# Optimization experiments

Measured on AMD Instinct MI355X. Metric: run time of the kernel, lower is better.

## Reference

```python
import jax, jax.numpy as jnp
import numpy as np

G = 4          # conv groups (hardcoded in module)
C = 1024       # channels (hardcoded cin=cout=1024)
SCALE = 1.0 / np.sqrt(1024.0).astype(np.float32)  # 1/sqrt(c/h), h=1


def grouped_proj(x, W, b):
    # pointwise grouped Conv1d == block-diagonal matmul over channel groups
    # x: [B, C, P], W: [G, C//G out, C//G in], b: [C]
    B, C_, P = x.shape
    xg = x.reshape(B, G, C_ // G, P)
    y = jnp.einsum('goi,bgip->bgop', W, xg)  # [B, G, C//G, P]
    return y.reshape(B, C_, P) + b[None, :, None]


def setup_inputs() -> dict:
    key = jax.random.key(0)
    ks = jax.random.split(key, 8)
    B, PK, PQ = 8, 1024, 4096
    cg = C // G
    w_std = 1.0 / np.sqrt(cg).astype(np.float32)  # ~ conv default init scale
    return {
        'Xq': jax.random.normal(ks[0], (B, C, PQ), jnp.float32),
        'Xk': jax.random.normal(ks[1], (B, C, PK), jnp.float32),
        'Wq': jax.random.normal(ks[2], (G, cg, cg), jnp.float32) * w_std,
        'bq': jax.random.normal(ks[3], (C,), jnp.float32) * 0.01,
        'Wk': jax.random.normal(ks[4], (G, cg, cg), jnp.float32) * w_std,
        'bk': jax.random.normal(ks[5], (C,), jnp.float32) * 0.01,
        'Wv': jax.random.normal(ks[6], (G, cg, cg), jnp.float32) * w_std,
        'bv': jax.random.normal(ks[7], (C,), jnp.float32) * 0.01,
    }


def reference(Xq, Xk, Wq, bq, Wk, bk, Wv, bv):
    # Q and K are both projected from Xk; V from Xq (as in the torch code)
    Q = grouped_proj(Xk, Wq, bq)   # [B, C, Pk]
    K = grouped_proj(Xk, Wk, bk)   # [B, C, Pk]
    V = grouped_proj(Xq, Wv, bv)   # [B, C, Pq]
    b, c, pk = K.shape
    pq = V.shape[-1]
    h = 1
    Qh = Q.reshape(b, h, c // h, pk)
    Kh = K.reshape(b, h, c // h, pk)
    Vh = V.reshape(b, h, c // h, pq)
    # H: [B, h, Pk, Pq], contraction over channels; softmax over dim=-2 (Pk)
    H = jnp.einsum('bhci,bhcj->bhij', Kh, Vh) * SCALE
    H = jax.nn.softmax(H, axis=-2)
    # sparse_constrain: Gram over last axis vs identity, mean squared error
    mid = jnp.einsum('bhci,bhki->bhck', H, H)          # [B, h, Pk, Pk]
    Iden = jnp.eye(pk, dtype=H.dtype)[None, None]       # broadcast over B, h
    sparse_loss = jnp.mean((mid - Iden) ** 2)
    # out: mix Q along Pk with attention H -> [B, h, C, Pq]
    out = jnp.einsum('bhij,bhki->bhkj', H, Qh).reshape(b, c, pq)
    return out, sparse_loss, H
```

## Files before the change

kernel.cpp:

```cpp
#include <hip/hip_runtime.h>

typedef _Float16 f16;
typedef f16 f16x4 __attribute__((ext_vector_type(4)));
typedef f16 f16x8 __attribute__((ext_vector_type(8)));
typedef float f32x4 __attribute__((ext_vector_type(4)));

__device__ __forceinline__ void gload16(const void* g, void* ldsbase) {
  __builtin_amdgcn_global_load_lds((const __attribute__((address_space(1))) unsigned int*)g,
                                   (__attribute__((address_space(3))) unsigned int*)ldsbase, 16, 0, 0);
}

__device__ __forceinline__ int swz(int row, int c) {
  return row * 64 + ((c ^ ((row >> 1) & 3)) << 4);
}

template<int MODE>
__global__ void __launch_bounds__(512, 2)
gemm256(const f16* __restrict__ A, const f16* __restrict__ Bm, float* __restrict__ Cf,
        f16* __restrict__ E16, f16* __restrict__ E16t,
        int K, long sA, long sB, float scale, float* __restrict__ aux) {
  __shared__ f16 sb[65536];
  const int t = threadIdx.x, l = t & 63, w = t >> 6;
  const int wr = w >> 2, wc = w & 3;
  const int bid = blockIdx.x;
  const int swzb = (bid & 7) * 64 + (bid >> 3);
  const long b = swzb >> 6;
  const int inner = swzb & 63;
  const int bx = inner >> 2, by = inner & 3;
  const char* Abyte = (const char*)(A + b * sA + (long)(by * 256) * K);
  const char* Bbyte = (const char*)(Bm + b * sB + (long)(bx * 256) * K);

  int offSrc[4];
#pragma unroll
  for (int i = 0; i < 4; ++i) {
    int cid = i * 512 + t, row = cid >> 3, slot = cid & 7;
    offSrc[i] = row * (K * 2) + ((slot ^ (row & 7)) << 4);
  }
  int offAf[8][2], offBf[4][2];
#pragma unroll
  for (int mi = 0; mi < 8; ++mi) {
    int r = wr * 128 + mi * 16 + (l & 15);
#pragma unroll
    for (int ks = 0; ks < 2; ++ks)
      offAf[mi][ks] = r * 64 + ((((ks << 2) + (l >> 4)) ^ (r & 7)) << 3);
  }
#pragma unroll
  for (int ni = 0; ni < 4; ++ni) {
    int r = wc * 64 + ni * 16 + (l & 15);
#pragma unroll
    for (int ks = 0; ks < 2; ++ks)
      offBf[ni][ks] = r * 64 + ((((ks << 2) + (l >> 4)) ^ (r & 7)) << 3);
  }

  const int NT = K >> 6;
  f32x4 acc[8][4] = {};

  auto STAGE = [&](int kt, int bsel) {
    f16* la = sb + bsel * 32768;
    f16* lb = la + 16384;
    const char* as = Abyte + (long)kt * 128;
    const char* bs = Bbyte + (long)kt * 128;
#pragma unroll
    for (int i = 0; i < 4; ++i)
      gload16(as + offSrc[i], la + (i * 512 + (w << 6)) * 8);
#pragma unroll
    for (int i = 0; i < 4; ++i)
      gload16(bs + offSrc[i], lb + (i * 512 + (w << 6)) * 8);
  };

  STAGE(0, 0);
  for (int kt = 0; kt < NT; ++kt) {
    const int cur = kt & 1;
    if (kt + 1 < NT) {
      STAGE(kt + 1, cur ^ 1);
      asm volatile("s_waitcnt vmcnt(8)" ::: "memory");
    } else {
      asm volatile("s_waitcnt vmcnt(0)" ::: "memory");
    }
    __builtin_amdgcn_s_barrier();
    asm volatile("" ::: "memory");
    const f16* la = sb + cur * 32768;
    const f16* lb = la + 16384;
#pragma unroll
    for (int ks = 0; ks < 2; ++ks) {
      f16x8 bf[4];
#pragma unroll
      for (int ni = 0; ni < 4; ++ni) bf[ni] = *(const f16x8*)(lb + offBf[ni][ks]);
#pragma unroll
      for (int mi = 0; mi < 8; ++mi) {
        f16x8 af = *(const f16x8*)(la + offAf[mi][ks]);
#pragma unroll
        for (int ni = 0; ni < 4; ++ni)
          acc[mi][ni] = __builtin_amdgcn_mfma_f32_16x16x32_f16(af, bf[ni], acc[mi][ni], 0, 0, 0);
      }
    }
    asm volatile("s_waitcnt lgkmcnt(0)" ::: "memory");
    __builtin_amdgcn_s_barrier();
    asm volatile("" ::: "memory");
  }

  const int i0 = by * 256, j0 = bx * 256;
  if (MODE == 2) {
    float csum[4] = {};
#pragma unroll
    for (int mi = 0; mi < 8; ++mi)
#pragma unroll
      for (int ni = 0; ni < 4; ++ni)
#pragma unroll
        for (int q = 0; q < 4; ++q) {
          float e = __expf(acc[mi][ni][q] * scale);
          acc[mi][ni][q] = e;
          csum[ni] += e;
        }
#pragma unroll
    for (int ni = 0; ni < 4; ++ni) {
      csum[ni] += __shfl_xor(csum[ni], 16);
      csum[ni] += __shfl_xor(csum[ni], 32);
    }
    float* colp = (float*)(sb + 34816);
    if (l < 16) {
#pragma unroll
      for (int ni = 0; ni < 4; ++ni) colp[wr * 256 + wc * 64 + ni * 16 + l] = csum[ni];
    }
    __syncthreads();
    if (t < 256) aux[(b * 4 + by) * 4096 + bx * 256 + t] = colp[t] + colp[256 + t];
    f16* E16b = E16 + b * 4194304L;
    f16* E16tb = E16t + b * 4194304L;
#pragma unroll
    for (int s = 0; s < 4; ++s) {
      if (wr == (s >> 1)) {
        const int h = s & 1;
#pragma unroll
        for (int m2 = 0; m2 < 4; ++m2)
#pragma unroll
          for (int ni = 0; ni < 4; ++ni)
#pragma unroll
            for (int q = 0; q < 4; ++q)
              sb[(m2 * 16 + (l >> 4) * 4 + q) * 264 + wc * 64 + ni * 16 + (l & 15)] =
                  (f16)acc[h * 4 + m2][ni][q];
      }
      __syncthreads();
#pragma unroll
      for (int ii = 0; ii < 4; ++ii) {
        int cid = ii * 512 + t, r = cid >> 5, cc = cid & 31;
        *(f16x8*)(E16b + (long)(i0 + s * 64 + r) * 4096 + j0 + cc * 8) =
            *(const f16x8*)(sb + r * 264 + cc * 8);
      }
      const int q4 = w >> 1, r8 = l >> 3, ic = l & 7;
#pragma unroll
      for (int ii = 0; ii < 4; ++ii) {
        int j = q4 * 64 + r8 * 8 + (w & 1) * 4 + ii;
        f16x8 v;
#pragma unroll
        for (int k2 = 0; k2 < 8; ++k2) v[k2] = sb[(ic * 8 + k2) * 264 + j];
        *(f16x8*)(E16tb + (long)(j0 + j) * 1024 + i0 + s * 64 + ic * 8) = v;
      }
      __syncthreads();
    }
  }
}

__global__ void __launch_bounds__(512, 2)
fused3(const f16* __restrict__ Q, const f16* __restrict__ Et, float* __restrict__ Cf,
       const float* __restrict__ invg,
       const f16* __restrict__ E, const f16* __restrict__ inv2sg,
       float* __restrict__ Hf, float* __restrict__ parts) {
  __shared__ f16 sb[69632];
  const int t = threadIdx.x, l = t & 63, w = t >> 6;
  const int wr = w >> 2, wc = w & 3;

  if (blockIdx.x < 80) {
    const int bid = blockIdx.x;
    const long b = bid & 7;
    int by = 0, r = bid >> 3;
    while (r >= 4 - by) { r -= 4 - by; ++by; }
    const int bx = by + r;
    const char* Abyte = (const char*)(E + b * 4194304L + (long)(by * 256) * 4096);
    const char* Bbyte = (const char*)(E + b * 4194304L + (long)(bx * 256) * 4096);
    f16* invl = sb + 65536;
    gload16((const char*)(inv2sg + b * 4096) + (long)t * 16, invl + (w << 6) * 8);
    int offSrc[4];
#pragma unroll
    for (int i = 0; i < 4; ++i) {
      int cid = i * 512 + t, row = cid >> 3, slot = cid & 7;
      offSrc[i] = row * 8192 + ((slot ^ (row & 7)) << 4);
    }
    int offAf[8][2], offBf[4][2];
#pragma unroll
    for (int mi = 0; mi < 8; ++mi) {
      int rr = wr * 128 + mi * 16 + (l & 15);
#pragma unroll
      for (int ks = 0; ks < 2; ++ks)
        offAf[mi][ks] = rr * 64 + ((((ks << 2) + (l >> 4)) ^ (rr & 7)) << 3);
    }
#pragma unroll
    for (int ni = 0; ni < 4; ++ni) {
      int rr = wc * 64 + ni * 16 + (l & 15);
#pragma unroll
      for (int ks = 0; ks < 2; ++ks)
        offBf[ni][ks] = rr * 64 + ((((ks << 2) + (l >> 4)) ^ (rr & 7)) << 3);
    }
    f32x4 acc[8][4] = {};
    auto STAGE = [&](int kt, int bsel) {
      f16* la = sb + bsel * 32768;
      f16* lb = la + 16384;
      const char* as = Abyte + (long)kt * 128;
      const char* bs = Bbyte + (long)kt * 128;
#pragma unroll
      for (int i = 0; i < 4; ++i) gload16(as + offSrc[i], la + (i * 512 + (w << 6)) * 8);
#pragma unroll
      for (int i = 0; i < 4; ++i) gload16(bs + offSrc[i], lb + (i * 512 + (w << 6)) * 8);
    };
    const int kwA = bx * 16;
    const int kwB = by * 16;
    const bool dual = (by != bx);
    STAGE(0, 0);
    for (int kt = 0; kt < 64; ++kt) {
      const int cur = kt & 1;
      if (kt + 1 < 64) {
        STAGE(kt + 1, cur ^ 1);
        const int pk = kt - 1;
        const bool wrote = (pk >= kwA && pk < kwA + 16) || (dual && pk >= kwB && pk < kwB + 16);
        if (wrote) asm volatile("s_waitcnt vmcnt(40)" ::: "memory");
        else       asm volatile("s_waitcnt vmcnt(8)" ::: "memory");
      } else {
        asm volatile("s_waitcnt vmcnt(0)" ::: "memory");
      }
      __builtin_amdgcn_s_barrier();
      asm volatile("" ::: "memory");
      const f16* la = sb + cur * 32768;
      const f16* lb = la + 16384;
#pragma unroll
      for (int ks = 0; ks < 2; ++ks) {
        const f16x8 invv = *(const f16x8*)(invl + kt * 64 + ks * 32 + ((l >> 4) << 3));
        f16x8 bf[4];
#pragma unroll
        for (int ni = 0; ni < 4; ++ni) bf[ni] = *(const f16x8*)(lb + offBf[ni][ks]);
#pragma unroll
        for (int mi = 0; mi < 8; ++mi) {
          f16x8 af = *(const f16x8*)(la + offAf[mi][ks]) * invv;
#pragma unroll
          for (int ni = 0; ni < 4; ++ni)
            acc[mi][ni] = __builtin_amdgcn_mfma_f32_16x16x32_f16(af, bf[ni], acc[mi][ni], 0, 0, 0);
        }
      }
      if (kt >= kwA && kt < kwA + 16) {
        const float iv = sqrtf((float)invl[kt * 64 + l]) * (1.0f / 64.0f);
        float* hp = Hf + b * 4194304L + (long)(by * 256 + w * 32) * 4096 + kt * 64 + l;
#pragma unroll
        for (int rr = 0; rr < 32; ++rr) {
          const int row = w * 32 + rr;
          f16 ev = la[row * 64 + ((((l >> 3) ^ (row & 7)) << 3) | (l & 7))];
          hp[(long)rr * 4096] = (float)ev * iv;
        }
      }
      if (dual && kt >= kwB && kt < kwB + 16) {
        const float iv = sqrtf((float)invl[kt * 64 + l]) * (1.0f / 64.0f);
        float* hp = Hf + b * 4194304L + (long)(bx * 256 + w * 32) * 4096 + kt * 64 + l;
#pragma unroll
        for (int rr = 0; rr < 32; ++rr) {
          const int row = w * 32 + rr;
          f16 ev = lb[row * 64 + ((((l >> 3) ^ (row & 7)) << 3) | (l & 7))];
          hp[(long)rr * 4096] = (float)ev * iv;
        }
      }
      asm volatile("s_waitcnt lgkmcnt(0)" ::: "memory");
      __builtin_amdgcn_s_barrier();
      asm volatile("" ::: "memory");
    }
    const int gr0 = by * 256 + wr * 128 + (l >> 4) * 4;
    const int gc0 = bx * 256 + wc * 64 + (l & 15);
    float p = 0.f;
#pragma unroll
    for (int mi = 0; mi < 8; ++mi)
#pragma unroll
      for (int ni = 0; ni < 4; ++ni)
#pragma unroll
        for (int q = 0; q < 4; ++q) {
          float e = acc[mi][ni][q] * (1.0f / 4096.0f);
          if (gr0 + mi * 16 + q == gc0 + ni * 16) e -= 1.f;
          p += e * e;
        }
    if (dual) p *= 2.f;
#pragma unroll
    for (int d = 32; d; d >>= 1) p += __shfl_down(p, d);
    __shared__ float red[8];
    if (l == 0) red[w] = p;
    __syncthreads();
    if (t == 0) {
      float s = 0.f;
#pragma unroll
      for (int i = 0; i < 8; ++i) s += red[i];
      parts[bid] = s;
    }
  } else {
    const int bid = blockIdx.x - 80;
    const int swzb = (bid & 7) * 64 + (bid >> 3);
    const long b = swzb >> 6;
    const int inner = swzb & 63;
    const int bx = inner >> 2, by = inner & 3;
    const char* Abyte = (const char*)(Q + b * 1048576L + (long)(by * 256) * 1024);
    const char* Bbyte = (const char*)(Et + b * 4194304L + (long)(bx * 256) * 1024);
    int offSrc[4];
#pragma unroll
    for (int i = 0; i < 4; ++i) {
      int cid = i * 512 + t, row = cid >> 3, slot = cid & 7;
      offSrc[i] = row * 2048 + ((slot ^ (row & 7)) << 4);
    }
    int offAf[8][2], offBf[4][2];
#pragma unroll
    for (int mi = 0; mi < 8; ++mi) {
      int r = wr * 128 + mi * 16 + (l & 15);
#pragma unroll
      for (int ks = 0; ks < 2; ++ks)
        offAf[mi][ks] = r * 64 + ((((ks << 2) + (l >> 4)) ^ (r & 7)) << 3);
    }
#pragma unroll
    for (int ni = 0; ni < 4; ++ni) {
      int r = wc * 64 + ni * 16 + (l & 15);
#pragma unroll
      for (int ks = 0; ks < 2; ++ks)
        offBf[ni][ks] = r * 64 + ((((ks << 2) + (l >> 4)) ^ (r & 7)) << 3);
    }
    f32x4 acc[8][4] = {};
    auto STAGE = [&](int kt, int bsel) {
      f16* la = sb + bsel * 32768;
      f16* lb = la + 16384;
      const char* as = Abyte + (long)kt * 128;
      const char* bs = Bbyte + (long)kt * 128;
#pragma unroll
      for (int i = 0; i < 4; ++i) gload16(as + offSrc[i], la + (i * 512 + (w << 6)) * 8);
#pragma unroll
      for (int i = 0; i < 4; ++i) gload16(bs + offSrc[i], lb + (i * 512 + (w << 6)) * 8);
    };
    STAGE(0, 0);
    for (int kt = 0; kt < 16; ++kt) {
      const int cur = kt & 1;
      if (kt + 1 < 16) {
        STAGE(kt + 1, cur ^ 1);
        asm volatile("s_waitcnt vmcnt(8)" ::: "memory");
      } else {
        asm volatile("s_waitcnt vmcnt(0)" ::: "memory");
      }
      __builtin_amdgcn_s_barrier();
      asm volatile("" ::: "memory");
      const f16* la = sb + cur * 32768;
      const f16* lb = la + 16384;
#pragma unroll
      for (int ks = 0; ks < 2; ++ks) {
        f16x8 bf[4];
#pragma unroll
        for (int ni = 0; ni < 4; ++ni) bf[ni] = *(const f16x8*)(lb + offBf[ni][ks]);
#pragma unroll
        for (int mi = 0; mi < 8; ++mi) {
          f16x8 af = *(const f16x8*)(la + offAf[mi][ks]);
#pragma unroll
          for (int ni = 0; ni < 4; ++ni)
            acc[mi][ni] = __builtin_amdgcn_mfma_f32_16x16x32_f16(af, bf[ni], acc[mi][ni], 0, 0, 0);
        }
      }
      asm volatile("s_waitcnt lgkmcnt(0)" ::: "memory");
      __builtin_amdgcn_s_barrier();
      asm volatile("" ::: "memory");
    }
    const float* ip = invg + b * 4096 + bx * 256 + wc * 64;
    float iv[4];
#pragma unroll
    for (int ni = 0; ni < 4; ++ni) iv[ni] = ip[ni * 16 + (l & 15)];
    float* Cb = Cf + b * 4194304L + (long)(by * 256 + wr * 128) * 4096 + bx * 256 + wc * 64;
#pragma unroll
    for (int mi = 0; mi < 8; ++mi)
#pragma unroll
      for (int ni = 0; ni < 4; ++ni)
#pragma unroll
        for (int q = 0; q < 4; ++q)
          Cb[(long)(mi * 16 + (l >> 4) * 4 + q) * 4096 + ni * 16 + (l & 15)] = acc[mi][ni][q] * iv[ni];
  }
}

__global__ void __launch_bounds__(512)
proj_qk(const float* __restrict__ X, const f16* __restrict__ Wq16, const f16* __restrict__ Wk16,
        const float* __restrict__ bq, const float* __restrict__ bk,
        f16* __restrict__ Q, f16* __restrict__ Kt) {
  __shared__ f16 sb[20480];
  f16* Wqs = sb;
  f16* Wks = sb + 8192;
  f16* Xs = sb + 16384;
  const int t = threadIdx.x, l = t & 63, w = t >> 6;
  const int wrq = w >> 1, wcq = w & 1;
  const int bg = blockIdx.z, g = bg & 3;
  const long b = bg >> 2;
  const int p0 = blockIdx.x * 128;
  const float* Xb = X + b * 1048576 + (long)g * 262144;
  const char* WqB = (const char*)(Wq16 + g * 65536);
  const char* WkB = (const char*)(Wk16 + g * 65536);
  int wOff[2];
#pragma unroll
  for (int i = 0; i < 2; ++i) {
    int c = i * 512 + t, row = c >> 2, slot = (c & 3) ^ ((row >> 1) & 3);
    wOff[i] = row * 512 + (slot << 4);
  }
  const int xp = t & 127, xc = t >> 7;
  const float* xS = Xb + (long)(xc * 8) * 1024 + p0 + xp;
  const int xo = swz(xp, xc);
  int offW[4], offX[4];
#pragma unroll
  for (int i = 0; i < 4; ++i) {
    int rc = wrq * 64 + i * 16 + (l & 15);
    offW[i] = swz(rc, l >> 4);
    int rp = wcq * 64 + i * 16 + (l & 15);
    offX[i] = swz(rp, l >> 4);
  }
  f32x4 accq[4][4] = {}, acck[4][4] = {};
  for (int k0 = 0; k0 < 256; k0 += 32) {
#pragma unroll
    for (int i = 0; i < 2; ++i) {
      gload16(WqB + wOff[i] + k0 * 2, Wqs + (i * 512 + (w << 6)) * 8);
      gload16(WkB + wOff[i] + k0 * 2, Wks + (i * 512 + (w << 6)) * 8);
    }
    const float* xs = xS + (long)k0 * 1024;
    f16x8 v;
#pragma unroll
    for (int d = 0; d < 8; ++d) v[d] = (f16)xs[(long)d * 1024];
    *(f16x8*)((char*)Xs + xo) = v;
    __syncthreads();
    f16x8 qf[4], kf[4], xf[4];
#pragma unroll
    for (int i = 0; i < 4; ++i) {
      qf[i] = *(const f16x8*)((const char*)Wqs + offW[i]);
      kf[i] = *(const f16x8*)((const char*)Wks + offW[i]);
      xf[i] = *(const f16x8*)((const char*)Xs + offX[i]);
    }
#pragma unroll
    for (int mi = 0; mi < 4; ++mi)
#pragma unroll
      for (int ni = 0; ni < 4; ++ni) {
        accq[mi][ni] = __builtin_amdgcn_mfma_f32_16x16x32_f16(qf[mi], xf[ni], accq[mi][ni], 0, 0, 0);
        acck[ni][mi] = __builtin_amdgcn_mfma_f32_16x16x32_f16(xf[ni], kf[mi], acck[ni][mi], 0, 0, 0);
      }
    __syncthreads();
  }
  f16* Qb = Q + b * 1048576 + (long)(g * 256 + wrq * 64) * 1024 + p0 + wcq * 64;
#pragma unroll
  for (int mi = 0; mi < 4; ++mi)
#pragma unroll
    for (int q = 0; q < 4; ++q) {
      float bv = bq[g * 256 + wrq * 64 + mi * 16 + (l >> 4) * 4 + q];
#pragma unroll
      for (int ni = 0; ni < 4; ++ni)
        Qb[(long)(mi * 16 + (l >> 4) * 4 + q) * 1024 + ni * 16 + (l & 15)] = (f16)(accq[mi][ni][q] + bv);
    }
  f16* Kb = Kt + b * 1048576 + (long)(p0 + wcq * 64) * 1024 + g * 256 + wrq * 64;
  float bcol[4];
#pragma unroll
  for (int ni = 0; ni < 4; ++ni) bcol[ni] = bk[g * 256 + wrq * 64 + ni * 16 + (l & 15)];
#pragma unroll
  for (int mi = 0; mi < 4; ++mi)
#pragma unroll
    for (int q = 0; q < 4; ++q)
#pragma unroll
      for (int ni = 0; ni < 4; ++ni)
        Kb[(long)(mi * 16 + (l >> 4) * 4 + q) * 1024 + ni * 16 + (l & 15)] = (f16)(acck[mi][ni][q] + bcol[ni]);
}

__global__ void __launch_bounds__(512)
proj_v(const float* __restrict__ X, const f16* __restrict__ Wv16, const float* __restrict__ bv,
       f16* __restrict__ Vt) {
  __shared__ f16 sb[12288];
  f16* Wvs = sb;
  f16* Xs = sb + 8192;
  const int t = threadIdx.x, l = t & 63, w = t >> 6;
  const int wrq = w >> 1, wcq = w & 1;
  const int bg = blockIdx.z, g = bg & 3;
  const long b = bg >> 2;
  const int p0 = blockIdx.x * 128;
  const float* Xb = X + b * 4194304 + (long)g * 1048576;
  const char* WvB = (const char*)(Wv16 + g * 65536);
  int wOff[2];
#pragma unroll
  for (int i = 0; i < 2; ++i) {
    int c = i * 512 + t, row = c >> 2, slot = (c & 3) ^ ((row >> 1) & 3);
    wOff[i] = row * 512 + (slot << 4);
  }
  const int xp = t & 127, xc = t >> 7;
  const float* xS = Xb + (long)(xc * 8) * 4096 + p0 + xp;
  const int xo = swz(xp, xc);
  int offW[4], offX[4];
#pragma unroll
  for (int i = 0; i < 4; ++i) {
    int rc = wrq * 64 + i * 16 + (l & 15);
    offW[i] = swz(rc, l >> 4);
    int rp = wcq * 64 + i * 16 + (l & 15);
    offX[i] = swz(rp, l >> 4);
  }
  f32x4 acc[4][4] = {};
  for (int k0 = 0; k0 < 256; k0 += 32) {
#pragma unroll
    for (int i = 0; i < 2; ++i)
      gload16(WvB + wOff[i] + k0 * 2, Wvs + (i * 512 + (w << 6)) * 8);
    const float* xs = xS + (long)k0 * 4096;
    f16x8 v;
#pragma unroll
    for (int d = 0; d < 8; ++d) v[d] = (f16)xs[(long)d * 4096];
    *(f16x8*)((char*)Xs + xo) = v;
    __syncthreads();
    f16x8 wf[4], xf[4];
#pragma unroll
    for (int i = 0; i < 4; ++i) {
      wf[i] = *(const f16x8*)((const char*)Wvs + offW[i]);
      xf[i] = *(const f16x8*)((const char*)Xs + offX[i]);
    }
#pragma unroll
    for (int mi = 0; mi < 4; ++mi)
#pragma unroll
      for (int ni = 0; ni < 4; ++ni)
        acc[mi][ni] = __builtin_amdgcn_mfma_f32_16x16x32_f16(xf[mi], wf[ni], acc[mi][ni], 0, 0, 0);
    __syncthreads();
  }
  f16* Vb = Vt + b * 4194304 + (long)(p0 + wcq * 64) * 1024 + g * 256 + wrq * 64;
  float bcol[4];
#pragma unroll
  for (int ni = 0; ni < 4; ++ni) bcol[ni] = bv[g * 256 + wrq * 64 + ni * 16 + (l & 15)];
#pragma unroll
  for (int mi = 0; mi < 4; ++mi)
#pragma unroll
    for (int q = 0; q < 4; ++q)
#pragma unroll
      for (int ni = 0; ni < 4; ++ni)
        Vb[(long)(mi * 16 + (l >> 4) * 4 + q) * 1024 + ni * 16 + (l & 15)] = (f16)(acc[mi][ni][q] + bcol[ni]);
}

__global__ void __launch_bounds__(256)
inv_k(const float* __restrict__ colsum, float* __restrict__ inv, f16* __restrict__ inv2s) {
  int gid = blockIdx.x * 256 + threadIdx.x;
  int b = gid >> 12, j = gid & 4095;
  const float* cp = colsum + (long)(b * 4) * 4096 + j;
  float s = 0.f;
#pragma unroll
  for (int my = 0; my < 4; ++my) s += cp[my * 4096];
  float iv = 1.f / s;
  inv[gid] = iv;
  inv2s[gid] = (f16)(iv * iv * 4096.0f);
}

__global__ void cvt3(const float* __restrict__ a, const float* __restrict__ b2,
                     const float* __restrict__ c, f16* __restrict__ da,
                     f16* __restrict__ db, f16* __restrict__ dc) {
  int i = blockIdx.x * 256 + threadIdx.x;
  int which = i >> 18, r = i & 262143;
  if (which == 0) da[r] = (f16)a[r];
  else if (which == 1) db[r] = (f16)b2[r];
  else dc[r] = (f16)c[r];
}

__global__ void __launch_bounds__(256)
finalize_k(const float* __restrict__ parts, float* __restrict__ o) {
  const int t = threadIdx.x;
  float s = (t < 80) ? parts[t] : 0.f;
#pragma unroll
  for (int d = 32; d; d >>= 1) s += __shfl_down(s, d);
  __shared__ float red[4];
  if ((t & 63) == 0) red[t >> 6] = s;
  __syncthreads();
  if (t == 0) *o = (red[0] + red[1] + red[2] + red[3]) * (1.0f / 8388608.0f);
}

extern "C" void kernel_launch(void* const* d_in, const int* in_sizes, int n_in,
                              void* d_out, int out_size, void* d_ws, size_t ws_size,
                              hipStream_t stream) {
  const float* Xq = (const float*)d_in[0];
  const float* Xk = (const float*)d_in[1];
  const float* Wq = (const float*)d_in[2];
  const float* bq = (const float*)d_in[3];
  const float* Wk = (const float*)d_in[4];
  const float* bk = (const float*)d_in[5];
  const float* Wv = (const float*)d_in[6];
  const float* bv = (const float*)d_in[7];
  float* out = (float*)d_out;
  float* loss_out = out + 33554432;
  float* Hf = out + 33554433;

  char* ws = (char*)d_ws;
  f16* W16q = (f16*)(ws);
  f16* W16k = (f16*)(ws + (1 << 19));
  f16* W16v = (f16*)(ws + 2L * (1 << 19));
  f16* Q16  = (f16*)(ws + 3L * (1 << 19));
  f16* Kt16 = (f16*)(ws + 3L * (1 << 19) + (1L << 24));
  f16* Vt16 = (f16*)(ws + 3L * (1 << 19) + 2L * (1 << 24));
  f16* E16  = (f16*)(ws + 3L * (1 << 19) + 2L * (1 << 24) + (1L << 26));
  f16* E16t = (f16*)(ws + 3L * (1 << 19) + 2L * (1 << 24) + 2L * (1 << 26));
  char* tail = ws + 3L * (1 << 19) + 2L * (1 << 24) + 3L * (1 << 26);
  float* parts = (float*)tail;
  float* invb  = (float*)(tail + 8192);
  f16*   inv2s = (f16*)(tail + 8192 + 131072);
  float* colsum = (float*)(ws);

  cvt3<<<3072, 256, 0, stream>>>(Wq, Wk, Wv, W16q, W16k, W16v);

  proj_qk<<<dim3(8, 1, 32), 512, 0, stream>>>(Xk, W16q, W16k, bq, bk, Q16, Kt16);
  proj_v <<<dim3(32, 1, 32), 512, 0, stream>>>(Xq, W16v, bv, Vt16);

  gemm256<2><<<512, 512, 0, stream>>>(Kt16, Vt16, nullptr, E16, E16t,
      1024, 1L << 20, 1L << 22, 0.03125f, colsum);

  inv_k<<<128, 256, 0, stream>>>(colsum, invb, inv2s);

  fused3<<<592, 512, 0, stream>>>(Q16, E16t, out, invb, E16, inv2s, Hf, parts);
  finalize_k<<<1, 256, 0, stream>>>(parts, loss_out);
}
```

Before: 379.8 us.

## Split Gram GEMM K dimension in two and reduce partial tiles separately

The sparse-loss Gram GEMM blocks in the fused kernel now split the 4096-long reduction into two halves, doubling Gram blocks from 80 to 160 so the long-running tail blocks are shorter and load balance with the output GEMM blocks improves. Each half writes its full 256x256 fp32 partial tile to workspace, and a new gram_red kernel sums the halves, subtracts identity and reduces squared error. The H write-out schedule is remapped so each panel is still written exactly once. This adds about 42MB of extra global traffic and one more kernel launch.

Result: faster. 371.3 us, median of 2 (-2.2%).

```diff
diff --git a/kernel.cpp b/kernel.cpp
--- a/kernel.cpp
+++ b/kernel.cpp
@@ -164,19 +164,24 @@
 fused3(const f16* __restrict__ Q, const f16* __restrict__ Et, float* __restrict__ Cf,
        const float* __restrict__ invg,
        const f16* __restrict__ E, const f16* __restrict__ inv2sg,
-       float* __restrict__ Hf, float* __restrict__ parts) {
+       float* __restrict__ Hf, float* __restrict__ midS) {
   __shared__ f16 sb[69632];
   const int t = threadIdx.x, l = t & 63, w = t >> 6;
   const int wr = w >> 2, wc = w & 3;
 
-  if (blockIdx.x < 80) {
+  if (blockIdx.x < 160) {
     const int bid = blockIdx.x;
     const long b = bid & 7;
-    int by = 0, r = bid >> 3;
+    const int rest = bid >> 3;
+    const int h = rest & 1;
+    int by = 0, r = rest >> 1;
     while (r >= 4 - by) { r -= 4 - by; ++by; }
     const int bx = by + r;
-    const char* Abyte = (const char*)(E + b * 4194304L + (long)(by * 256) * 4096);
-    const char* Bbyte = (const char*)(E + b * 4194304L + (long)(bx * 256) * 4096);
+    const char* Abyte = (const char*)(E + b * 4194304L + (long)(by * 256) * 4096 + 2048L * h);
+    const char* Bbyte = (const char*)(E + b * 4194304L + (long)(bx * 256) * 4096 + 2048L * h);
+    const int d = bx - by;
+    const int wA = (d == 1) ? 0 : (d == 2 ? 1 : -1);
+    const int wB = (d == 3) ? 0 : ((d == 1 && by >= 1) ? 1 : -1);
     f16* invl = sb + 65536;
     gload16((const char*)(inv2sg + b * 4096) + (long)t * 16, invl + (w << 6) * 8);
     int offSrc[4];
@@ -201,26 +206,23 @@
         offBf[ni][ks] = rr * 64 + ((((ks << 2) + (l >> 4)) ^ (rr & 7)) << 3);
     }
     f32x4 acc[8][4] = {};
-    auto STAGE = [&](int kt, int bsel) {
+    auto STAGE = [&](int lk, int bsel) {
       f16* la = sb + bsel * 32768;
       f16* lb = la + 16384;
-      const char* as = Abyte + (long)kt * 128;
-      const char* bs = Bbyte + (long)kt * 128;
+      const char* as = Abyte + (long)lk * 128;
+      const char* bs = Bbyte + (long)lk * 128;
 #pragma unroll
       for (int i = 0; i < 4; ++i) gload16(as + offSrc[i], la + (i * 512 + (w << 6)) * 8);
 #pragma unroll
       for (int i = 0; i < 4; ++i) gload16(bs + offSrc[i], lb + (i * 512 + (w << 6)) * 8);
     };
-    const int kwA = bx * 16;
-    const int kwB = by * 16;
-    const bool dual = (by != bx);
     STAGE(0, 0);
-    for (int kt = 0; kt < 64; ++kt) {
-      const int cur = kt & 1;
-      if (kt + 1 < 64) {
-        STAGE(kt + 1, cur ^ 1);
-        const int pk = kt - 1;
-        const bool wrote = (pk >= kwA && pk < kwA + 16) || (dual && pk >= kwB && pk < kwB + 16);
+    for (int lk = 0; lk < 32; ++lk) {
+      const int cur = lk & 1;
+      if (lk + 1 < 32) {
+        STAGE(lk + 1, cur ^ 1);
+        const int ps = (lk - 1) >> 4;
+        const bool wrote = (lk >= 1) && (wA == ps || wB == ps);
         if (wrote) asm volatile("s_waitcnt vmcnt(40)" ::: "memory");
         else       asm volatile("s_waitcnt vmcnt(8)" ::: "memory");
       } else {
@@ -228,11 +230,12 @@
       }
       __builtin_amdgcn_s_barrier();
       asm volatile("" ::: "memory");
+      const int ktg = 32 * h + lk;
       const f16* la = sb + cur * 32768;
       const f16* lb = la + 16384;
 #pragma unroll
       for (int ks = 0; ks < 2; ++ks) {
-        const f16x8 invv = *(const f16x8*)(invl + kt * 64 + ks * 32 + ((l >> 4) << 3));
+        const f16x8 invv = *(const f16x8*)(invl + ktg * 64 + ks * 32 + ((l >> 4) << 3));
         f16x8 bf[4];
 #pragma unroll
         for (int ni = 0; ni < 4; ++ni) bf[ni] = *(const f16x8*)(lb + offBf[ni][ks]);
@@ -244,57 +247,34 @@
             acc[mi][ni] = __builtin_amdgcn_mfma_f32_16x16x32_f16(af, bf[ni], acc[mi][ni], 0, 0, 0);
         }
       }
-      if (kt >= kwA && kt < kwA + 16) {
-        const float iv = sqrtf((float)invl[kt * 64 + l]) * (1.0f / 64.0f);
-        float* hp = Hf + b * 4194304L + (long)(by * 256 + w * 32) * 4096 + kt * 64 + l;
-#pragma unroll
-        for (int rr = 0; rr < 32; ++rr) {
-          const int row = w * 32 + rr;
-          f16 ev = la[row * 64 + ((((l >> 3) ^ (row & 7)) << 3) | (l & 7))];
-          hp[(long)rr * 4096] = (float)ev * iv;
-        }
-      }
-      if (dual && kt >= kwB && kt < kwB + 16) {
-        const float iv = sqrtf((float)invl[kt * 64 + l]) * (1.0f / 64.0f);
-        float* hp = Hf + b * 4194304L + (long)(bx * 256 + w * 32) * 4096 + kt * 64 + l;
-#pragma unroll
-        for (int rr = 0; rr < 32; ++rr) {
-          const int row = w * 32 + rr;
-          f16 ev = lb[row * 64 + ((((l >> 3) ^ (row & 7)) << 3) | (l & 7))];
-          hp[(long)rr * 4096] = (float)ev * iv;
+      const int slot = lk >> 4;
+      if (wA == slot || wB == slot) {
+        const int panel = (wA == slot) ? by : bx;
+        const f16* src = (wA == slot) ? la : lb;
+        const float iv = sqrtf((float)invl[ktg * 64 + l]) * (1.0f / 64.0f);
+        float* hp = Hf + b * 4194304L + (long)(panel * 256 + w * 32) * 4096 + ktg * 64 + l;
+#pragma unroll
+        for (int rr2 = 0; rr2 < 32; ++rr2) {
+          const int row = w * 32 + rr2;
+          f16 ev = src[row * 64 + ((((l >> 3) ^ (row & 7)) << 3) | (l & 7))];
+          hp[(long)rr2 * 4096] = (float)ev * iv;
         }
       }
       asm volatile("s_waitcnt lgkmcnt(0)" ::: "memory");
       __builtin_amdgcn_s_barrier();
       asm volatile("" ::: "memory");
     }
-    const int gr0 = by * 256 + wr * 128 + (l >> 4) * 4;
-    const int gc0 = bx * 256 + wc * 64 + (l & 15);
-    float p = 0.f;
+    float* mt = midS + (long)(((rest >> 1) * 8 + b) * 2 + h) * 65536;
 #pragma unroll
     for (int mi = 0; mi < 8; ++mi)
 #pragma unroll
       for (int ni = 0; ni < 4; ++ni)
 #pragma unroll
-        for (int q = 0; q < 4; ++q) {
-          float e = acc[mi][ni][q] * (1.0f / 4096.0f);
-          if (gr0 + mi * 16 + q == gc0 + ni * 16) e -= 1.f;
-          p += e * e;
-        }
-    if (dual) p *= 2.f;
-#pragma unroll
-    for (int d = 32; d; d >>= 1) p += __shfl_down(p, d);
-    __shared__ float red[8];
-    if (l == 0) red[w] = p;
-    __syncthreads();
-    if (t == 0) {
-      float s = 0.f;
-#pragma unroll
-      for (int i = 0; i < 8; ++i) s += red[i];
-      parts[bid] = s;
-    }
+        for (int q = 0; q < 4; ++q)
+          mt[(wr * 128 + mi * 16 + (l >> 4) * 4 + q) * 256 + wc * 64 + ni * 16 + (l & 15)] =
+              acc[mi][ni][q];
   } else {
-    const int bid = blockIdx.x - 80;
+    const int bid = blockIdx.x - 160;
     const int swzb = (bid & 7) * 64 + (bid >> 3);
     const long b = swzb >> 6;
     const int inner = swzb & 63;
@@ -376,6 +356,31 @@
         for (int q = 0; q < 4; ++q)
           Cb[(long)(mi * 16 + (l >> 4) * 4 + q) * 4096 + ni * 16 + (l & 15)] = acc[mi][ni][q] * iv[ni];
   }
+}
+
+__global__ void __launch_bounds__(256)
+gram_red(const float* __restrict__ midS, float* __restrict__ parts) {
+  const int tile = blockIdx.x, ck = blockIdx.y, t = threadIdx.x;
+  int by = 0, r = tile >> 3;
+  while (r >= 4 - by) { r -= 4 - by; ++by; }
+  const int bx = by + r;
+  const bool diag = (by == bx);
+  const float* m0 = midS + (long)(tile * 2) * 65536 + ck * 8192;
+  const float* m1 = m0 + 65536;
+  float p = 0.f;
+  for (int i = t; i < 8192; i += 256) {
+    int gi = ck * 8192 + i;
+    float e = (m0[i] + m1[i]) * (1.0f / 4096.0f);
+    if (diag && (gi >> 8) == (gi & 255)) e -= 1.f;
+    p += e * e;
+  }
+  if (!diag) p *= 2.f;
+#pragma unroll
+  for (int d2 = 32; d2; d2 >>= 1) p += __shfl_down(p, d2);
+  __shared__ float red[4];
+  if ((t & 63) == 0) red[t >> 6] = p;
+  __syncthreads();
+  if (t == 0) parts[tile * 8 + ck] = red[0] + red[1] + red[2] + red[3];
 }
 
 __global__ void __launch_bounds__(512)
@@ -556,7 +561,8 @@
 __global__ void __launch_bounds__(256)
 finalize_k(const float* __restrict__ parts, float* __restrict__ o) {
   const int t = threadIdx.x;
-  float s = (t < 80) ? parts[t] : 0.f;
+  float s = 0.f;
+  for (int i = t; i < 640; i += 256) s += parts[i];
 #pragma unroll
   for (int d = 32; d; d >>= 1) s += __shfl_down(s, d);
   __shared__ float red[4];
@@ -593,6 +599,7 @@
   float* parts = (float*)tail;
   float* invb  = (float*)(tail + 8192);
   f16*   inv2s = (f16*)(tail + 8192 + 131072);
+  float* midS  = (float*)(tail + 8192 + 131072 + 65536);
   float* colsum = (float*)(ws);
 
   cvt3<<<3072, 256, 0, stream>>>(Wq, Wk, Wv, W16q, W16k, W16v);
@@ -605,6 +612,8 @@
 
   inv_k<<<128, 256, 0, stream>>>(colsum, invb, inv2s);
 
-  fused3<<<592, 512, 0, stream>>>(Q16, E16t, out, invb, E16, inv2s, Hf, parts);
+  fused3<<<672, 512, 0, stream>>>(Q16, E16t, out, invb, E16, inv2s, Hf, midS);
+
+  gram_red<<<dim3(80, 8), 256, 0, stream>>>(midS, parts);
   finalize_k<<<1, 256, 0, stream>>>(parts, loss_out);
 }
```
